# Performance work log

Hardware: AMD Instinct MI355X
Metric: run time of the kernel (lower is better)

## Reference

```python
import jax, jax.numpy as jnp
import numpy as np

REG_LAMBDA = 1e-07


def setup_inputs() -> dict:
    key = jax.random.key(0)
    k1, k2, k3 = jax.random.split(key, 3)
    B, C, H, W = 2, 3, 512, 512
    return {
        "input_image": jax.random.uniform(k1, (B, C, H, W), jnp.float32),
        "guide_image": jax.random.uniform(k2, (B, H, W), jnp.float32),
        "output_image": jax.random.uniform(k3, (B, C, H, W), jnp.float32),
    }


def _bgu_fit(input_image, guide_image, output_image, reg_lambda=REG_LAMBDA):
    B, C, H, W = input_image.shape
    out_ch = output_image.shape[1]
    gh, gw, gd = round(H / 16), round(W / 16), 16  # default grid_size path
    Ca = C + 1
    G = gh * gw * gd
    dt = input_image.dtype

    inp = jnp.moveaxis(input_image, 1, -1)      # [B,H,W,C]
    outp = jnp.moveaxis(output_image, 1, -1)    # [B,H,W,out_ch]
    input_aug = jnp.concatenate([inp, jnp.ones((B, H, W, 1), dt)], -1)  # [B,H,W,Ca]

    ys = jnp.arange(H, dtype=dt)
    xs = jnp.arange(W, dtype=dt)
    gx = jnp.broadcast_to(((xs + 0.5) * (gw - 1) / W)[None, None, :], (B, H, W))
    gy = jnp.broadcast_to(((ys + 0.5) * (gh - 1) / H)[None, :, None], (B, H, W))
    gz = guide_image * (gd - 1)

    x0 = jnp.clip(jnp.floor(gx).astype(jnp.int32), 0, gw - 1)
    y0 = jnp.clip(jnp.floor(gy).astype(jnp.int32), 0, gh - 1)
    z0 = jnp.clip(jnp.floor(gz).astype(jnp.int32), 0, gd - 1)
    x1 = jnp.minimum(x0 + 1, gw - 1)
    y1 = jnp.minimum(y0 + 1, gh - 1)
    z1 = jnp.minimum(z0 + 1, gd - 1)
    wx = gx - x0.astype(dt)
    wy = gy - y0.astype(dt)
    wz = gz - z0.astype(dt)

    N = H * W
    flat = lambda a: a.reshape(B, N)
    x0f, x1f, y0f, y1f, z0f, z1f = map(flat, (x0, x1, y0, y1, z0, z1))
    wxf, wyf, wzf = map(flat, (wx, wy, wz))

    x_stack = jnp.stack([x0f, x0f, x0f, x0f, x1f, x1f, x1f, x1f], -1)
    y_stack = jnp.stack([y0f, y0f, y1f, y1f, y0f, y0f, y1f, y1f], -1)
    z_stack = jnp.stack([z0f, z1f, z0f, z1f, z0f, z1f, z0f, z1f], -1)
    w_stack = jnp.stack([
        (1 - wxf) * (1 - wyf) * (1 - wzf),
        (1 - wxf) * (1 - wyf) * wzf,
        (1 - wxf) * wyf * (1 - wzf),
        (1 - wxf) * wyf * wzf,
        wxf * (1 - wyf) * (1 - wzf),
        wxf * (1 - wyf) * wzf,
        wxf * wyf * (1 - wzf),
        wxf * wyf * wzf,
    ], -1)  # [B,N,8]

    linear_idx = y_stack * (gw * gd) + x_stack * gd + z_stack  # [B,N,8]

    ia = input_aug.reshape(B, N, Ca)
    ob = outp.reshape(B, N, out_ch)
    # weight_image defaults to ones -> contrib equals the trilinear weights
    outer_alpha = jnp.einsum('bni,bnj->bnij', ia, ia)           # [B,N,Ca,Ca]
    outer_beta = jnp.einsum('bnk,bnj->bnkj', ob, ia)            # [B,N,out_ch,Ca]
    alpha_vals = w_stack[..., None, None] * outer_alpha[:, :, None]  # [B,N,8,Ca,Ca]
    beta_vals = w_stack[..., None, None] * outer_beta[:, :, None]    # [B,N,8,out_ch,Ca]

    # scatter-add splat into the bilateral grid (batch offset trick)
    idx = (linear_idx + (jnp.arange(B, dtype=jnp.int32) * G)[:, None, None]).reshape(-1)
    S = jnp.zeros((B * G, Ca, Ca), dt).at[idx].add(alpha_vals.reshape(-1, Ca, Ca)).reshape(B, G, Ca, Ca)
    T = jnp.zeros((B * G, out_ch, Ca), dt).at[idx].add(beta_vals.reshape(-1, out_ch, Ca)).reshape(B, G, out_ch, Ca)

    counts = S[..., -1, -1]                                     # [B,G]
    wl = reg_lambda * (counts + 1.0)
    S_reg = S + wl[..., None, None] * jnp.eye(Ca, dtype=dt)

    # reg_T = True branch: bias T toward a per-cell gain-only affine model
    S_sum = S.sum(1)                                            # [B,Ca,Ca]
    T_sum = T.sum(1)                                            # [B,out_ch,Ca]
    wlg = reg_lambda * (counts.sum(1) + 1.0)                    # [B]
    gain_global = T_sum[:, :, 3] / (S_sum[:, :-1, 3] + wlg[:, None])   # [B,out_ch]
    gain_global = jnp.broadcast_to(gain_global[:, None], (B, G, out_ch))
    gain_local = T[..., :, 3] / (S[..., :-1, 3] + wl[..., None])       # [B,G,out_ch]
    mixed_gain = jnp.where((counts == 0)[..., None], gain_global, gain_local)
    diag = jnp.eye(out_ch, dtype=dt) * mixed_gain[..., None, :]        # diag_embed: [B,G,out_ch,out_ch]
    default_gamma = jnp.concatenate([diag, jnp.zeros((B, G, out_ch, Ca - out_ch), dt)], -1)
    T_reg = T + wl[..., None, None] * default_gamma

    # gamma = solve(S^T, T^T)^T, matching the torch permute/solve/permute
    gamma = jnp.swapaxes(
        jnp.linalg.solve(jnp.swapaxes(S_reg, -1, -2), jnp.swapaxes(T_reg, -1, -2)),
        -1, -2)
    return gamma.reshape(B, gh, gw, gd, out_ch, Ca).astype(jnp.float32)


def reference(input_image, guide_image, output_image):
    return _bgu_fit(input_image, guide_image, output_image)
```

## Files before the change

kernel.cpp:

```cpp
#include <hip/hip_runtime.h>

#define HH 512
#define WW 512
#define HWN (HH*WW)
#define GH 32
#define GW 32
#define GD 16
#define NB 2
#define NBIN 15
#define CAP 125
#define PLN 1156

__device__ __forceinline__ float row16_red(float x) {
    int t;
    t = __builtin_amdgcn_update_dpp(0, __builtin_bit_cast(int, x), 0x111, 0xf, 0xf, true);
    x += __builtin_bit_cast(float, t);
    t = __builtin_amdgcn_update_dpp(0, __builtin_bit_cast(int, x), 0x112, 0xf, 0xf, true);
    x += __builtin_bit_cast(float, t);
    t = __builtin_amdgcn_update_dpp(0, __builtin_bit_cast(int, x), 0x114, 0xf, 0xf, true);
    x += __builtin_bit_cast(float, t);
    t = __builtin_amdgcn_update_dpp(0, __builtin_bit_cast(int, x), 0x118, 0xf, 0xf, true);
    x += __builtin_bit_cast(float, t);
    return x;
}

__global__ __launch_bounds__(256) void bgu_kernel(
    const float* __restrict__ inp, const float* __restrict__ guide,
    const float* __restrict__ outp, float* __restrict__ gamma)
{
    __shared__ float pl[7][PLN];
    __shared__ int rec[NBIN*CAP];
    __shared__ int cnt[16];

    int orig = blockIdx.x;
    int wg = (orig & 7) * (NB*GH*GW/8) + (orig >> 3);
    int cx = wg & (GW-1);
    int cy = (wg >> 5) & (GH-1);
    int b  = wg >> 10;

    int tid  = threadIdx.x;
    int lane = tid & 63;
    int wv   = tid >> 6;

    if (tid < 16) cnt[tid] = 0;
    __syncthreads();

    int xlo = (cx <= 1) ? 0 : ((1024*(cx-1) - 31)/62 + 1);
    int xhi = min(WW-1, (1024*(cx+1) - 32)/62);
    int ylo = (cy <= 1) ? 0 : ((1024*(cy-1) - 31)/62 + 1);
    int yhi = min(HH-1, (1024*(cy+1) - 32)/62);
    int nx = xhi - xlo + 1;

    const float* inb = inp  + (size_t)b*3*HWN;
    const float* onb = outp + (size_t)b*3*HWN;
    const float* gb  = guide + (size_t)b*HWN;

    const float SC = 31.0f / 512.0f;

    {
        int q = 256 / nx;
        int r = 256 - q * nx;
        int dy = tid / nx;
        int y = ylo + dy;
        int x = xlo + tid - dy * nx;
        int il = tid;

        while (y <= yhi) {
            int pix = (y << 9) | x;
            float g = gb[pix];
            pl[0][il] = inb[pix];
            pl[1][il] = inb[HWN  + pix];
            pl[2][il] = inb[2*HWN+ pix];
            pl[3][il] = onb[pix];
            pl[4][il] = onb[HWN  + pix];
            pl[5][il] = onb[2*HWN+ pix];
            pl[6][il] = g;
            int z0 = min((int)(g * 15.0f), NBIN-1);
            int idx = atomicAdd(&cnt[z0], 1);
            if (idx < CAP)
                rec[z0*CAP + idx] = il | ((x - xlo) << 11) | ((y - ylo) << 17);
            x += r; y += q; il += 256;
            if (x > xhi) { x -= nx; ++y; }
        }
    }
    __syncthreads();

    int bin  = (wv << 2) | (lane >> 4);
    int slot = lane & 15;
    int n = (bin < NBIN) ? min(cnt[bin], CAP) : 0;

    float aA[22], aB[22];
    #pragma unroll
    for (int f = 0; f < 22; ++f) { aA[f] = 0.0f; aB[f] = 0.0f; }

    float binf = (float)bin;
    #pragma unroll 2
    for (int e = slot; e < n; e += 16) {
        unsigned rc = (unsigned)rec[bin*CAP + e];
        int il = rc & 2047;
        int x = xlo + ((rc >> 11) & 63);
        int y = ylo + (int)(rc >> 17);
        float v0 = pl[0][il], v1 = pl[1][il], v2 = pl[2][il];
        float o0 = pl[3][il], o1 = pl[4][il], o2 = pl[5][il];
        float g  = pl[6][il];
        float gxv = ((float)x + 0.5f) * SC;
        int   x0 = (int)gxv;
        float wx = gxv - (float)x0;
        float wxc = (x0 == cx) ? (1.0f - wx) : wx;
        float gyv = ((float)y + 0.5f) * SC;
        int   y0 = (int)gyv;
        float wy = gyv - (float)y0;
        float wyc = (y0 == cy) ? (1.0f - wy) : wy;
        float w2 = wxc * wyc;
        float gz = g * 15.0f;
        float wz = gz - binf;
        float wA = w2 * (1.0f - wz);
        float wB = w2 * wz;
        {
            float s0 = wA*v0, s1 = wA*v1, s2 = wA*v2;
            aA[0] = fmaf(s0, v0, aA[0]);  aA[1] = fmaf(s0, v1, aA[1]);
            aA[2] = fmaf(s0, v2, aA[2]);  aA[3] += s0;
            aA[4] = fmaf(s1, v1, aA[4]);  aA[5] = fmaf(s1, v2, aA[5]);
            aA[6] += s1;
            aA[7] = fmaf(s2, v2, aA[7]);  aA[8] += s2;  aA[9] += wA;
            float t0 = wA*o0, t1 = wA*o1, t2 = wA*o2;
            aA[10] = fmaf(t0, v0, aA[10]); aA[11] = fmaf(t0, v1, aA[11]);
            aA[12] = fmaf(t0, v2, aA[12]); aA[13] += t0;
            aA[14] = fmaf(t1, v0, aA[14]); aA[15] = fmaf(t1, v1, aA[15]);
            aA[16] = fmaf(t1, v2, aA[16]); aA[17] += t1;
            aA[18] = fmaf(t2, v0, aA[18]); aA[19] = fmaf(t2, v1, aA[19]);
            aA[20] = fmaf(t2, v2, aA[20]); aA[21] += t2;
        }
        {
            float s0 = wB*v0, s1 = wB*v1, s2 = wB*v2;
            aB[0] = fmaf(s0, v0, aB[0]);  aB[1] = fmaf(s0, v1, aB[1]);
            aB[2] = fmaf(s0, v2, aB[2]);  aB[3] += s0;
            aB[4] = fmaf(s1, v1, aB[4]);  aB[5] = fmaf(s1, v2, aB[5]);
            aB[6] += s1;
            aB[7] = fmaf(s2, v2, aB[7]);  aB[8] += s2;  aB[9] += wB;
            float t0 = wB*o0, t1 = wB*o1, t2 = wB*o2;
            aB[10] = fmaf(t0, v0, aB[10]); aB[11] = fmaf(t0, v1, aB[11]);
            aB[12] = fmaf(t0, v2, aB[12]); aB[13] += t0;
            aB[14] = fmaf(t1, v0, aB[14]); aB[15] = fmaf(t1, v1, aB[15]);
            aB[16] = fmaf(t1, v2, aB[16]); aB[17] += t1;
            aB[18] = fmaf(t2, v0, aB[18]); aB[19] = fmaf(t2, v1, aB[19]);
            aB[20] = fmaf(t2, v2, aB[20]); aB[21] += t2;
        }
    }
    __syncthreads();

    float* sc = (float*)pl;
    #pragma unroll
    for (int f = 0; f < 22; ++f) {
        float sa = row16_red(aA[f]);
        float sb = row16_red(aB[f]);
        if ((lane & 15) == 15) {
            sc[(bin*2 + 0)*24 + f] = sa;
            sc[(bin*2 + 1)*24 + f] = sb;
        }
    }
    __syncthreads();

    if (tid < GD) {
        int c = tid;
        float av[22];
        #pragma unroll
        for (int f = 0; f < 22; ++f) {
            float s = sc[(c*2 + 0)*24 + f];
            if (c > 0) s += sc[((c-1)*2 + 1)*24 + f];
            av[f] = s;
        }

        float Sf[4][4];
        {
            int p = 0;
            for (int i = 0; i < 4; ++i)
                for (int j = i; j < 4; ++j) { Sf[i][j] = av[p]; Sf[j][i] = av[p]; ++p; }
        }
        float Tf[3][4];
        for (int k = 0; k < 3; ++k)
            for (int j = 0; j < 4; ++j) Tf[k][j] = av[10 + k*4 + j];

        float counts = Sf[3][3];
        float wl = 1e-7f * (counts + 1.0f);

        float gout[3];
        #pragma unroll
        for (int k = 0; k < 3; ++k)
            gout[k] = Tf[k][3] / (Sf[k][3] + wl);

        double A[4][4], Bm[4][3];
        for (int i = 0; i < 4; ++i)
            for (int j = 0; j < 4; ++j)
                A[i][j] = (double)Sf[i][j] + ((i == j) ? (double)wl : 0.0);
        for (int j = 0; j < 4; ++j)
            for (int k = 0; k < 3; ++k) {
                double t = (double)Tf[k][j];
                if (j == k) t += (double)wl * (double)gout[k];
                Bm[j][k] = t;
            }

        double inv[4];
        #pragma unroll
        for (int col = 0; col < 4; ++col) {
            inv[col] = 1.0 / A[col][col];
            #pragma unroll
            for (int r2 = col+1; r2 < 4; ++r2) {
                double f = A[r2][col] * inv[col];
                #pragma unroll
                for (int j = col; j < 4; ++j) A[r2][j] -= f * A[col][j];
                #pragma unroll
                for (int k = 0; k < 3; ++k) Bm[r2][k] -= f * Bm[col][k];
            }
        }
        double G[4][3];
        #pragma unroll
        for (int r2 = 3; r2 >= 0; --r2) {
            #pragma unroll
            for (int k = 0; k < 3; ++k) {
                double s2 = Bm[r2][k];
                for (int j = r2+1; j < 4; ++j) s2 -= A[r2][j] * G[j][k];
                G[r2][k] = s2 * inv[r2];
            }
        }

        size_t cell = (((size_t)b*GH + cy)*GW + cx)*GD + c;
        float* op = gamma + cell * 12;
        #pragma unroll
        for (int k = 0; k < 3; ++k)
            #pragma unroll
            for (int j = 0; j < 4; ++j)
                op[k*4 + j] = (float)G[j][k];
    }
}

extern "C" void kernel_launch(void* const* d_in, const int* in_sizes, int n_in,
                              void* d_out, int out_size, void* d_ws, size_t ws_size,
                              hipStream_t stream) {
    const float* inp   = (const float*)d_in[0];
    const float* guide = (const float*)d_in[1];
    const float* outp  = (const float*)d_in[2];
    float* out = (float*)d_out;

    bgu_kernel<<<NB*GH*GW, 256, 0, stream>>>(inp, guide, outp, out);
}
```

Baseline: 83.04 us.

## Split lower/upper z-bin accumulation across lane parity to halve accumulator registers

Each 16-lane row previously had every lane accumulate both the lower-bin and upper-bin moment sums (44 registers). Now even lanes accumulate the lower-bin weight and odd lanes the upper-bin weight, with 8 pixel slots per bin. The DPP reduction drops its first shuffle step, so each parity sums separately. Launch bounds also request 8 blocks per multiprocessor. This cuts register pressure to raise occupancy, but each lane now does the per-pixel loads and weight math for twice as many pixels, so that work is duplicated across each lane pair.

New measurement: 82.60 us. No clear change (-0.5%).

```diff
diff --git a/kernel.cpp b/kernel.cpp
--- a/kernel.cpp
+++ b/kernel.cpp
@@ -11,10 +11,8 @@
 #define CAP 125
 #define PLN 1156
 
-__device__ __forceinline__ float row16_red(float x) {
+__device__ __forceinline__ float parity_row_red(float x) {
     int t;
-    t = __builtin_amdgcn_update_dpp(0, __builtin_bit_cast(int, x), 0x111, 0xf, 0xf, true);
-    x += __builtin_bit_cast(float, t);
     t = __builtin_amdgcn_update_dpp(0, __builtin_bit_cast(int, x), 0x112, 0xf, 0xf, true);
     x += __builtin_bit_cast(float, t);
     t = __builtin_amdgcn_update_dpp(0, __builtin_bit_cast(int, x), 0x114, 0xf, 0xf, true);
@@ -24,7 +22,7 @@
     return x;
 }
 
-__global__ __launch_bounds__(256) void bgu_kernel(
+__global__ __launch_bounds__(256, 8) void bgu_kernel(
     const float* __restrict__ inp, const float* __restrict__ guide,
     const float* __restrict__ outp, float* __restrict__ gamma)
 {
@@ -86,16 +84,17 @@
     __syncthreads();
 
     int bin  = (wv << 2) | (lane >> 4);
-    int slot = lane & 15;
+    int sel  = lane & 1;
+    int ps   = (lane & 15) >> 1;
     int n = (bin < NBIN) ? min(cnt[bin], CAP) : 0;
 
-    float aA[22], aB[22];
+    float acc[22];
     #pragma unroll
-    for (int f = 0; f < 22; ++f) { aA[f] = 0.0f; aB[f] = 0.0f; }
+    for (int f = 0; f < 22; ++f) acc[f] = 0.0f;
 
     float binf = (float)bin;
     #pragma unroll 2
-    for (int e = slot; e < n; e += 16) {
+    for (int e = ps; e < n; e += 8) {
         unsigned rc = (unsigned)rec[bin*CAP + e];
         int il = rc & 2047;
         int x = xlo + ((rc >> 11) & 63);
@@ -114,50 +113,31 @@
         float w2 = wxc * wyc;
         float gz = g * 15.0f;
         float wz = gz - binf;
-        float wA = w2 * (1.0f - wz);
-        float wB = w2 * wz;
-        {
-            float s0 = wA*v0, s1 = wA*v1, s2 = wA*v2;
-            aA[0] = fmaf(s0, v0, aA[0]);  aA[1] = fmaf(s0, v1, aA[1]);
-            aA[2] = fmaf(s0, v2, aA[2]);  aA[3] += s0;
-            aA[4] = fmaf(s1, v1, aA[4]);  aA[5] = fmaf(s1, v2, aA[5]);
-            aA[6] += s1;
-            aA[7] = fmaf(s2, v2, aA[7]);  aA[8] += s2;  aA[9] += wA;
-            float t0 = wA*o0, t1 = wA*o1, t2 = wA*o2;
-            aA[10] = fmaf(t0, v0, aA[10]); aA[11] = fmaf(t0, v1, aA[11]);
-            aA[12] = fmaf(t0, v2, aA[12]); aA[13] += t0;
-            aA[14] = fmaf(t1, v0, aA[14]); aA[15] = fmaf(t1, v1, aA[15]);
-            aA[16] = fmaf(t1, v2, aA[16]); aA[17] += t1;
-            aA[18] = fmaf(t2, v0, aA[18]); aA[19] = fmaf(t2, v1, aA[19]);
-            aA[20] = fmaf(t2, v2, aA[20]); aA[21] += t2;
-        }
-        {
-            float s0 = wB*v0, s1 = wB*v1, s2 = wB*v2;
-            aB[0] = fmaf(s0, v0, aB[0]);  aB[1] = fmaf(s0, v1, aB[1]);
-            aB[2] = fmaf(s0, v2, aB[2]);  aB[3] += s0;
-            aB[4] = fmaf(s1, v1, aB[4]);  aB[5] = fmaf(s1, v2, aB[5]);
-            aB[6] += s1;
-            aB[7] = fmaf(s2, v2, aB[7]);  aB[8] += s2;  aB[9] += wB;
-            float t0 = wB*o0, t1 = wB*o1, t2 = wB*o2;
-            aB[10] = fmaf(t0, v0, aB[10]); aB[11] = fmaf(t0, v1, aB[11]);
-            aB[12] = fmaf(t0, v2, aB[12]); aB[13] += t0;
-            aB[14] = fmaf(t1, v0, aB[14]); aB[15] = fmaf(t1, v1, aB[15]);
-            aB[16] = fmaf(t1, v2, aB[16]); aB[17] += t1;
-            aB[18] = fmaf(t2, v0, aB[18]); aB[19] = fmaf(t2, v1, aB[19]);
-            aB[20] = fmaf(t2, v2, aB[20]); aB[21] += t2;
-        }
+        float w = sel ? (w2 * wz) : (w2 * (1.0f - wz));
+
+        float s0 = w*v0, s1 = w*v1, s2 = w*v2;
+        acc[0] = fmaf(s0, v0, acc[0]);  acc[1] = fmaf(s0, v1, acc[1]);
+        acc[2] = fmaf(s0, v2, acc[2]);  acc[3] += s0;
+        acc[4] = fmaf(s1, v1, acc[4]);  acc[5] = fmaf(s1, v2, acc[5]);
+        acc[6] += s1;
+        acc[7] = fmaf(s2, v2, acc[7]);  acc[8] += s2;  acc[9] += w;
+        float t0 = w*o0, t1 = w*o1, t2 = w*o2;
+        acc[10] = fmaf(t0, v0, acc[10]); acc[11] = fmaf(t0, v1, acc[11]);
+        acc[12] = fmaf(t0, v2, acc[12]); acc[13] += t0;
+        acc[14] = fmaf(t1, v0, acc[14]); acc[15] = fmaf(t1, v1, acc[15]);
+        acc[16] = fmaf(t1, v2, acc[16]); acc[17] += t1;
+        acc[18] = fmaf(t2, v0, acc[18]); acc[19] = fmaf(t2, v1, acc[19]);
+        acc[20] = fmaf(t2, v2, acc[20]); acc[21] += t2;
     }
     __syncthreads();
 
     float* sc = (float*)pl;
     #pragma unroll
     for (int f = 0; f < 22; ++f) {
-        float sa = row16_red(aA[f]);
-        float sb = row16_red(aB[f]);
-        if ((lane & 15) == 15) {
-            sc[(bin*2 + 0)*24 + f] = sa;
-            sc[(bin*2 + 1)*24 + f] = sb;
-        }
+        float s = parity_row_red(acc[f]);
+        int lr = lane & 15;
+        if (lr >= 14)
+            sc[(bin*2 + (lr & 1))*24 + f] = s;
     }
     __syncthreads();
 
```
